# Kernel tuning notes

Measured on AMD Instinct MI355X. Metric: run time of the kernel, lower is better.

The kernel has to match this reference:

```python
import jax, jax.numpy as jnp
import numpy as np

N, E, C, H, W = 5000, 80000, 32, 8, 8


def setup_inputs() -> dict:
    key = jax.random.key(0)
    k1, k2, k3, k4, k5, k6 = jax.random.split(key, 6)
    h = jax.random.normal(k1, (N, C, H, W), dtype=jnp.float32)
    e = jax.random.uniform(k2, (E,), dtype=jnp.float32)
    src = jax.random.randint(k3, (E,), 0, N, dtype=jnp.int32)
    # ensure every node receives at least one message (avoids -inf segments),
    # matching a connected graph where update_all covers all nodes
    dst = jnp.concatenate([jnp.arange(N, dtype=jnp.int32),
                           jax.random.randint(k4, (E - N,), 0, N, dtype=jnp.int32)])
    fan_in = C * 3 * 3
    bound = float(1.0 / np.sqrt(fan_in))
    conv_w = jax.random.uniform(k5, (C, C, 3, 3), minval=-bound, maxval=bound, dtype=jnp.float32)
    conv_b = jax.random.uniform(k6, (C,), minval=-bound, maxval=bound, dtype=jnp.float32)
    return {"h": h, "e": e, "conv_w": conv_w, "conv_b": conv_b, "src": src, "dst": dst}


def reference(h, e, conv_w, conv_b, src, dst):
    # message: gather source features per edge, scale by scalar edge weight
    m = e[:, None, None, None] * h[src]                      # [E, C, H, W]
    # conv2d(dim->dim, k=3, pad=1) + exact GELU, edges as batch dim
    m = jax.lax.conv_general_dilated(
        m, conv_w, window_strides=(1, 1), padding='SAME',
        dimension_numbers=('NCHW', 'OIHW', 'NCHW'))
    m = jax.nn.gelu(m + conv_b[None, :, None, None], approximate=False)
    # reduce: ragged max over each destination node's mailbox
    out = jax.ops.segment_max(m, dst, num_segments=h.shape[0])  # [N, C, H, W]
    return out
```

## Files before the change

### kernel.cpp

```cpp
#include <hip/hip_runtime.h>
#include <math.h>

#define CCH   32
#define HWPIX 64
#define CHW   2048
#define NHALF 2500
#define HT_STRIDE 40
#define HT_NODE   2600

typedef __attribute__((ext_vector_type(8))) short bf16x8;
typedef __attribute__((ext_vector_type(4))) float f32x4;
typedef __fp16 fp16x2 __attribute__((ext_vector_type(2)));
typedef unsigned int uint_t;
typedef unsigned short ushort_t;
typedef unsigned long long u64_t;

__device__ __forceinline__ ushort_t f2bf(float f) {
    uint_t u = __float_as_uint(f);
    u += 0x7fffu + ((u >> 16) & 1u);
    return (ushort_t)(u >> 16);
}

__device__ __forceinline__ uint_t pkh2(float a, float b) {
    fp16x2 p = __builtin_amdgcn_cvt_pkrtz(a, b);
    uint_t u;
    __builtin_memcpy(&u, &p, 4);
    return u;
}

__device__ __forceinline__ float h_lo(uint_t u) {
    ushort_t s = (ushort_t)u;
    __fp16 h;
    __builtin_memcpy(&h, &s, 2);
    return (float)h;
}
__device__ __forceinline__ float h_hi(uint_t u) { return h_lo(u >> 16); }

__device__ __forceinline__ float fgelu(float x) {
    float x2 = x * x;
    float t = x * fmaf(0.0713548162726f, x2, 1.5957691216f);
    float ez = __expf(-t);
    return x * __builtin_amdgcn_rcpf(1.0f + ez);
}

__global__ __launch_bounds__(256) void prep_kernel(
    int* __restrict__ cnt, int nn,
    const float* __restrict__ w, ushort_t* __restrict__ wfrag) {
    int t = threadIdx.x;
    if (blockIdx.x == 0) {
        for (int i = t; i < nn; i += 256) cnt[i] = 0;
    } else {
        for (int idx = t; idx < 18 * 64; idx += 256) {
            int ch = idx / (9 * 64);
            int rem = idx % (9 * 64);
            int tap = rem / 64;
            int l = rem % 64;
            int co = ch * 16 + (l & 15);
            int g = l >> 4;
            for (int j = 0; j < 8; j++) {
                int ci = g * 8 + j;
                wfrag[(size_t)idx * 8 + j] = f2bf(w[(co * CCH + ci) * 9 + tap]);
            }
        }
    }
}

__global__ __launch_bounds__(256) void scan_kernel(const int* __restrict__ cnt,
                                                   int* __restrict__ offs,
                                                   int* __restrict__ cursor,
                                                   int nn) {
    __shared__ int part[256];
    int t = threadIdx.x;
    int per = (nn + 255) >> 8;
    if (per > 32) per = 32;
    int base = t * per;
    int local[32];
    int sum = 0;
    for (int i = 0; i < per; i++) {
        int idx = base + i;
        int v = (idx < nn) ? cnt[idx] : 0;
        local[i] = sum;
        sum += v;
    }
    part[t] = sum;
    __syncthreads();
    int acc = sum;
    for (int d = 1; d < 256; d <<= 1) {
        int tv = (t >= d) ? part[t - d] : 0;
        __syncthreads();
        acc += tv;
        part[t] = acc;
        __syncthreads();
    }
    int excl = acc - sum;
    for (int i = 0; i < per; i++) {
        int idx = base + i;
        if (idx < nn) {
            int o = excl + local[i];
            offs[idx] = o;
            cursor[idx] = o;
        }
    }
    if (t == 255) offs[nn] = acc;
}

__global__ __launch_bounds__(256) void conv_hist_kernel(
    const float* __restrict__ h, const ushort_t* __restrict__ wfrag,
    ushort_t* __restrict__ convh, int nconv,
    const int* __restrict__ dst, int* cnt, int ne) {
    __shared__ ushort_t Ht[2 * HT_NODE];
    int b = blockIdx.x;
    int t = threadIdx.x;

    if (b >= nconv) {
        int i = (b - nconv) * 256 + t;
        if (i < ne) atomicAdd(&cnt[dst[i]], 1);
        return;
    }

    int node0 = b * 2;
    uint_t* Hd = (uint_t*)Ht;
#pragma unroll
    for (int nd = 0; nd < 2; nd++) {
        const float* hn = h + (size_t)(node0 + nd) * CHW;
#pragma unroll
        for (int it = 0; it < 4; it++) {
            int ci2 = it * 4 + (t >> 6);
            int p = t & 63;
            float a = hn[ci2 * 128 + p];
            float bb = hn[ci2 * 128 + 64 + p];
            uint_t val = (uint_t)f2bf(a) | ((uint_t)f2bf(bb) << 16);
            Hd[nd * (HT_NODE / 2) + p * (HT_STRIDE / 2) + ci2] = val;
        }
    }
    if (t < 40) Hd[0 * (HT_NODE / 2) + 64 * (HT_STRIDE / 2) + (t % 20)] = 0;
    if (t >= 40 && t < 80) Hd[1 * (HT_NODE / 2) + 64 * (HT_STRIDE / 2) + (t - 40) % 20] = 0;
    __syncthreads();

    int l = t & 63;
    int w = __builtin_amdgcn_readfirstlane(t >> 6);
    int nd = w >> 1;
    int ch = w & 1;
    int s = l & 15, g = l >> 4;
    int n = node0 + nd;

    bf16x8 A[9];
#pragma unroll
    for (int tap = 0; tap < 9; tap++)
        A[tap] = ((const bf16x8*)wfrag)[(ch * 9 + tap) * 64 + l];

    f32x4 C[4];
#pragma unroll
    for (int i = 0; i < 4; i++) C[i] = (f32x4){0.f, 0.f, 0.f, 0.f};

    const short* HtS = (const short*)(Ht + nd * HT_NODE);
#pragma unroll
    for (int tau = 0; tau < 4; tau++) {
        int p = tau * 16 + s;
        int y = p >> 3, x = p & 7;
#pragma unroll
        for (int tap = 0; tap < 9; tap++) {
            int dy = tap / 3 - 1, dx = tap % 3 - 1;
            int yy = y + dy, xx = x + dx;
            bool valid = (yy >= 0) & (yy < 8) & (xx >= 0) & (xx < 8);
            int pp = valid ? (yy * 8 + xx) : 64;
            bf16x8 B = *(const bf16x8*)&HtS[pp * HT_STRIDE + g * 8];
            C[tau] = __builtin_amdgcn_mfma_f32_16x16x32_bf16(A[tap], B, C[tau], 0, 0, 0);
        }
    }

    ushort_t* outn = convh + (size_t)n * CHW;
#pragma unroll
    for (int tau = 0; tau < 4; tau++) {
        uint2 v;
        v.x = pkh2(C[tau][0], C[tau][1]);
        v.y = pkh2(C[tau][2], C[tau][3]);
        *(uint2*)(outn + (tau * 16 + s) * 32 + ch * 16 + g * 4) = v;
    }
}

__global__ __launch_bounds__(256) void scatter_kernel(
    const int* __restrict__ dst, const int* __restrict__ src,
    const float* __restrict__ e, int* cursor, int2* __restrict__ swA, int ne) {
    int i = blockIdx.x * 256 + threadIdx.x;
    if (i < ne) {
        int p = atomicAdd(&cursor[dst[i]], 1);
        u64_t v = ((u64_t)(uint_t)__float_as_int(e[i]) << 32) | (uint_t)src[i];
        __builtin_nontemporal_store(v, (u64_t*)&swA[p]);
    }
}

__device__ __forceinline__ void red2h(uint_t* mn, uint_t* mx, uint_t d, uint_t w2) {
    uint_t v;
    asm("v_pk_mul_f16 %0, %1, %2" : "=v"(v) : "v"(d), "v"(w2));
    asm("v_pk_min_f16 %0, %0, %1" : "+v"(*mn) : "v"(v));
    asm("v_pk_max_f16 %0, %0, %1" : "+v"(*mx) : "v"(v));
}
__device__ __forceinline__ void red8h(uint_t* mn, uint_t* mx, uint4 qv, uint_t w2) {
    red2h(&mn[0], &mx[0], qv.x, w2);
    red2h(&mn[1], &mx[1], qv.y, w2);
    red2h(&mn[2], &mx[2], qv.z, w2);
    red2h(&mn[3], &mx[3], qv.w, w2);
}

__global__ __launch_bounds__(256) void gather_max_kernel(
    const ushort_t* __restrict__ convh, const float* __restrict__ bias,
    const int* __restrict__ offs, const int2* __restrict__ swA,
    float* __restrict__ out) {
    int t = threadIdx.x;
    int l = t & 63;
    int w = t >> 6;
    int b = blockIdx.x;
    int q = b & 3;
    int half = (b >> 2) & 1;
    int n = __builtin_amdgcn_readfirstlane(half * NHALF + (b >> 3) * 4 + w);
    int beg = offs[n], end = offs[n + 1];
    int last = end - 1;

    const char* qbase = (const char*)convh + 1024 * q + 16 * l;

    uint_t mn[4], mx[4];
#pragma unroll
    for (int i = 0; i < 4; i++) { mn[i] = 0x7c007c00u; mx[i] = 0xfc00fc00u; }

    uint4 D[8];
    uint_t Wh[8];
    int2 T[8];
#pragma unroll
    for (int k = 0; k < 8; k++) {
        int idx = beg + k; idx = idx < last ? idx : last;
        int2 d = swA[idx];
        D[k] = *(const uint4*)(qbase + (size_t)d.x * 4096);
        float wf = __int_as_float(d.y);
        Wh[k] = pkh2(wf, wf);
    }
#pragma unroll
    for (int k = 0; k < 8; k++) {
        int idx = beg + 8 + k; idx = idx < last ? idx : last;
        T[k] = swA[idx];
    }

    for (int j = beg; j < end; j += 8) {
        int2 U[8];
#pragma unroll
        for (int k = 0; k < 8; k++) {
            int idx = j + 16 + k; idx = idx < last ? idx : last;
            U[k] = swA[idx];
        }
#pragma unroll
        for (int k = 0; k < 8; k++) {
            red8h(mn, mx, D[k], Wh[k]);
            D[k] = *(const uint4*)(qbase + (size_t)T[k].x * 4096);
            float wf = __int_as_float(T[k].y);
            Wh[k] = pkh2(wf, wf);
        }
#pragma unroll
        for (int k = 0; k < 8; k++) T[k] = U[k];
    }

    const float4* b4 = (const float4*)(bias + (l & 3) * 8);
    float4 bLo = b4[0], bHi = b4[1];
    float bb[8] = {bLo.x, bLo.y, bLo.z, bLo.w, bHi.x, bHi.y, bHi.z, bHi.w};
    float* op = out + (size_t)n * CHW + (size_t)(l & 3) * 512 + q * 16 + (l >> 2);
#pragma unroll
    for (int k = 0; k < 4; k++) {
        float mx0 = h_lo(mx[k]), mx1 = h_hi(mx[k]);
        float mn0 = h_lo(mn[k]), mn1 = h_hi(mn[k]);
        float r0 = fmaxf(fgelu(mx0 + bb[2 * k]),     fgelu(mn0 + bb[2 * k]));
        float r1 = fmaxf(fgelu(mx1 + bb[2 * k + 1]), fgelu(mn1 + bb[2 * k + 1]));
        __builtin_nontemporal_store(r0, &op[(2 * k) * 64]);
        __builtin_nontemporal_store(r1, &op[(2 * k + 1) * 64]);
    }
}

extern "C" void kernel_launch(void* const* d_in, const int* in_sizes, int n_in,
                              void* d_out, int out_size, void* d_ws, size_t ws_size,
                              hipStream_t stream) {
    const float* h      = (const float*)d_in[0];
    const float* e      = (const float*)d_in[1];
    const float* conv_w = (const float*)d_in[2];
    const float* conv_b = (const float*)d_in[3];
    const int*   src    = (const int*)d_in[4];
    const int*   dst    = (const int*)d_in[5];
    int nn = in_sizes[0] / CHW;
    int ne = in_sizes[1];

    ushort_t* convh = (ushort_t*)d_ws;
    ushort_t* wfrag = convh + (size_t)nn * CHW;
    int*   cnt    = (int*)(wfrag + 18 * 64 * 8);
    int*   offs   = cnt + nn;
    int*   cursor = offs + nn + 2;
    int2*  swA    = (int2*)(cursor + nn);

    int nhist = (ne + 255) / 256;
    int nconv = nn / 2;

    prep_kernel<<<2, 256, 0, stream>>>(cnt, nn, conv_w, wfrag);
    conv_hist_kernel<<<nconv + nhist, 256, 0, stream>>>(
        h, wfrag, convh, nconv, dst, cnt, ne);
    scan_kernel<<<1, 256, 0, stream>>>(cnt, offs, cursor, nn);
    scatter_kernel<<<nhist, 256, 0, stream>>>(dst, src, e, cursor, swA, ne);
    gather_max_kernel<<<nn, 256, 0, stream>>>(convh, conv_b, offs, swA,
                                              (float*)d_out);
}
```

Measured before the change: 152.6 us.

## Assign gather work items per XCC via atomic queues for L2 locality

```diff
diff --git a/kernel.cpp b/kernel.cpp
--- a/kernel.cpp
+++ b/kernel.cpp
@@ -5,6 +5,7 @@
 #define HWPIX 64
 #define CHW   2048
 #define NHALF 2500
+#define NCHUNK 625
 #define HT_STRIDE 40
 #define HT_NODE   2600
 
@@ -44,11 +45,12 @@
 }
 
 __global__ __launch_bounds__(256) void prep_kernel(
-    int* __restrict__ cnt, int nn,
+    int* __restrict__ cnt, int nn, int* __restrict__ qcnt,
     const float* __restrict__ w, ushort_t* __restrict__ wfrag) {
     int t = threadIdx.x;
     if (blockIdx.x == 0) {
         for (int i = t; i < nn; i += 256) cnt[i] = 0;
+        if (t < 8) qcnt[t] = 0;
     } else {
         for (int idx = t; idx < 18 * 64; idx += 256) {
             int ch = idx / (9 * 64);
@@ -206,14 +208,31 @@
 __global__ __launch_bounds__(256) void gather_max_kernel(
     const ushort_t* __restrict__ convh, const float* __restrict__ bias,
     const int* __restrict__ offs, const int2* __restrict__ swA,
-    float* __restrict__ out) {
+    int* __restrict__ qcnt, float* __restrict__ out) {
+    __shared__ int s_item;
     int t = threadIdx.x;
+    if (t == 0) {
+        uint_t x;
+        asm volatile("s_getreg_b32 %0, hwreg(HW_REG_XCC_ID)" : "=s"(x));
+        x &= 7;
+        int item = -1;
+        for (int k = 0; k < 8; k++) {
+            int y = (int)((x + k) & 7);
+            int c = atomicAdd(&qcnt[y], 1);
+            if (c < NCHUNK) { item = y * NCHUNK + c; break; }
+        }
+        s_item = item;
+    }
+    __syncthreads();
+    int item = s_item;
+    if (item < 0) return;
+    int cls = item / NCHUNK;
+    int chunk = item % NCHUNK;
+    int q = cls & 3;
+    int half = cls >> 2;
     int l = t & 63;
     int w = t >> 6;
-    int b = blockIdx.x;
-    int q = b & 3;
-    int half = (b >> 2) & 1;
-    int n = __builtin_amdgcn_readfirstlane(half * NHALF + (b >> 3) * 4 + w);
+    int n = __builtin_amdgcn_readfirstlane(half * NHALF + chunk * 4 + w);
     int beg = offs[n], end = offs[n + 1];
     int last = end - 1;
 
@@ -291,15 +310,16 @@
     int*   offs   = cnt + nn;
     int*   cursor = offs + nn + 2;
     int2*  swA    = (int2*)(cursor + nn);
+    int*   qcnt   = (int*)(swA + ne);
 
     int nhist = (ne + 255) / 256;
     int nconv = nn / 2;
 
-    prep_kernel<<<2, 256, 0, stream>>>(cnt, nn, conv_w, wfrag);
+    prep_kernel<<<2, 256, 0, stream>>>(cnt, nn, qcnt, conv_w, wfrag);
     conv_hist_kernel<<<nconv + nhist, 256, 0, stream>>>(
         h, wfrag, convh, nconv, dst, cnt, ne);
     scan_kernel<<<1, 256, 0, stream>>>(cnt, offs, cursor, nn);
     scatter_kernel<<<nhist, 256, 0, stream>>>(dst, src, e, cursor, swA, ne);
     gather_max_kernel<<<nn, 256, 0, stream>>>(convh, conv_b, offs, swA,
-                                              (float*)d_out);
-}
+                                              qcnt, (float*)d_out);
+}
```

Result: slower. 180.4 us (+18.2%).
